# Performance work log

Hardware: AMD Instinct MI355X
Metric: run time of the kernel (lower is better)

## Reference

```python
import jax, jax.numpy as jnp
import numpy as np

EMBED_DIM = 768
NUM_HEADS = 12
HEAD_DIM = EMBED_DIM // NUM_HEADS


def setup_inputs() -> dict:
    key = jax.random.key(0)
    k_x, k_qkv_w, k_qkv_b, k_pw, k_pb = jax.random.split(key, 5)
    B, S = 16, 1024
    scale = 1.0 / np.sqrt(EMBED_DIM)
    return {
        "x": jax.random.normal(k_x, (B, S, EMBED_DIM), dtype=jnp.float32),
        "qkv_w": jax.random.normal(k_qkv_w, (EMBED_DIM, 3 * EMBED_DIM), dtype=jnp.float32) * scale,
        "qkv_b": jax.random.normal(k_qkv_b, (3 * EMBED_DIM,), dtype=jnp.float32) * 0.02,
        "proj_w": jax.random.normal(k_pw, (EMBED_DIM, EMBED_DIM), dtype=jnp.float32) * scale,
        "proj_b": jax.random.normal(k_pb, (EMBED_DIM,), dtype=jnp.float32) * 0.02,
    }


def reference(x, qkv_w, qkv_b, proj_w, proj_b):
    B, S, E = x.shape
    H, D = NUM_HEADS, HEAD_DIM
    qkv = x @ qkv_w + qkv_b                      # [B, S, 3E]
    qkv = qkv.reshape(B, S, 3, H, D)
    qkv = jnp.transpose(qkv, (2, 0, 3, 1, 4))    # [3, B, H, S, D]
    q, k, v = qkv[0], qkv[1], qkv[2]
    scores = jnp.einsum("bhqd,bhkd->bhqk", q, k) / jnp.sqrt(jnp.float32(D))
    probs = jax.nn.softmax(scores, axis=-1)      # dropout is identity in eval
    attn = jnp.einsum("bhqk,bhkd->bhqd", probs, v)
    attn = jnp.transpose(attn, (0, 2, 1, 3)).reshape(B, S, E)
    return attn @ proj_w + proj_b
```

## Files before the change

### kernel.cpp

```cpp
#include <hip/hip_runtime.h>
#include <hip/hip_bf16.h>

typedef unsigned short u16;
typedef short s16x8 __attribute__((ext_vector_type(8)));
typedef float f32x4 __attribute__((ext_vector_type(4)));

#define EMB 768
#define NH 12
#define HD 64
#define BB 16
#define SS 1024
#define MTOK (BB*SS)
#define NQKV (3*EMB)
#define QSZ ((size_t)BB*NH*SS*HD)

#define GLOBAL_AS const __attribute__((address_space(1))) void*
#define LDS_AS __attribute__((address_space(3))) void*

#if __has_builtin(__builtin_amdgcn_exp2f)
#define EXP2(x) __builtin_amdgcn_exp2f(x)
#else
#define EXP2(x) exp2f(x)
#endif

__device__ __forceinline__ u16 f2bf(float f){
  unsigned u = __float_as_uint(f);
  u += 0x7FFFu + ((u >> 16) & 1u);
  return (u16)(u >> 16);
}
__device__ __forceinline__ u16 f2bf_trunc(float f){
  return (u16)(__float_as_uint(f) >> 16);
}
__device__ __forceinline__ f32x4 mfma16(s16x8 a, s16x8 b, f32x4 c){
  return __builtin_amdgcn_mfma_f32_16x16x32_bf16(a, b, c, 0, 0, 0);
}

__global__ __launch_bounds__(256) void convert_f32_bf16(
    const float4* __restrict__ in, ushort4* __restrict__ out, int n4){
  int i = blockIdx.x * 256 + threadIdx.x;
  if(i < n4){
    float4 f = in[i];
    ushort4 o;
    o.x = f2bf(f.x); o.y = f2bf(f.y); o.z = f2bf(f.z); o.w = f2bf(f.w);
    out[i] = o;
  }
}

__global__ void transpose_conv(const float* __restrict__ in, u16* __restrict__ out,
                               int R, int C){
  __shared__ u16 tile[32][33];
  int bx = blockIdx.x * 32, by = blockIdx.y * 32;
  int tx = threadIdx.x & 31, ty = threadIdx.x >> 5;
  #pragma unroll
  for(int i = 0; i < 32; i += 8)
    tile[ty + i][tx] = f2bf(in[(size_t)(by + ty + i) * C + bx + tx]);
  __syncthreads();
  #pragma unroll
  for(int i = 0; i < 32; i += 8)
    out[(size_t)(bx + ty + i) * R + by + tx] = tile[tx][ty + i];
}

template<int MODE>
__global__ __launch_bounds__(256) void gemm_kernel(
    const u16* __restrict__ A, const u16* __restrict__ Bt,
    const float* __restrict__ bias,
    void* __restrict__ out0, u16* __restrict__ out1, u16* __restrict__ out2){
  const int K = 768;
  __shared__ u16 As[2][128*64];
  __shared__ u16 Bs[2][128*64];
  int tid = threadIdx.x;
  int m0 = blockIdx.y * 128, n0 = blockIdx.x * 128;
  int w = tid >> 6, lane = tid & 63, quad = lane >> 4, l15 = lane & 15;
  int wm = (w >> 1) * 64, wn = (w & 1) * 64;
  int rr = lane >> 3;
  int cp = lane & 7;
  f32x4 acc[4][4] = {};

  auto stage = [&](int p, int k0){
    #pragma unroll
    for(int it = 0; it < 4; ++it){
      int ci = it * 4 + w;
      int r  = ci * 8 + rr;
      int gc = (cp ^ (r & 7)) * 8;
      __builtin_amdgcn_global_load_lds(
          (GLOBAL_AS)(A + (size_t)(m0 + r) * K + k0 + gc),
          (LDS_AS)(As[p] + ci * 512 + lane * 8), 16, 0, 0);
      __builtin_amdgcn_global_load_lds(
          (GLOBAL_AS)(Bt + (size_t)(n0 + r) * K + k0 + gc),
          (LDS_AS)(Bs[p] + ci * 512 + lane * 8), 16, 0, 0);
    }
  };

  stage(0, 0);
  int p = 0;
  for(int k0 = 0; k0 < K; k0 += 64){
    __syncthreads();
    if(k0 + 64 < K) stage(p ^ 1, k0 + 64);
    #pragma unroll
    for(int kk = 0; kk < 2; kk++){
      s16x8 a[4], b[4];
      int ch = ((kk * 4 + quad) ^ (l15 & 7)) * 8;
      #pragma unroll
      for(int i = 0; i < 4; i++){
        a[i] = *(const s16x8*)&As[p][(wm + i*16 + l15) * 64 + ch];
        b[i] = *(const s16x8*)&Bs[p][(wn + i*16 + l15) * 64 + ch];
      }
      #pragma unroll
      for(int mt = 0; mt < 4; mt++)
        #pragma unroll
        for(int nt = 0; nt < 4; nt++)
          acc[mt][nt] = mfma16(a[mt], b[nt], acc[mt][nt]);
    }
    p ^= 1;
  }

  #pragma unroll
  for(int mt = 0; mt < 4; mt++){
    #pragma unroll
    for(int nt = 0; nt < 4; nt++){
      int n = n0 + wn + nt*16 + l15;
      float bv = bias[n];
      #pragma unroll
      for(int r = 0; r < 4; r++){
        int m = m0 + wm + mt*16 + quad*4 + r;
        float v = acc[mt][nt][r] + bv;
        if(MODE == 1){
          ((float*)out0)[(size_t)m * EMB + n] = v;
        } else {
          u16 hv = f2bf(v);
          int which = n / EMB, rem = n - which * EMB;
          int h = rem >> 6, d = rem & 63;
          int b = m >> 10, s = m & 1023;
          size_t bh = (size_t)(b * NH + h);
          if(which == 0)      ((u16*)out0)[(bh * SS + s) * HD + d] = hv;
          else if(which == 1) out1[(bh * SS + s) * HD + d] = hv;
          else                out2[(bh * HD + d) * SS + s] = hv;
        }
      }
    }
  }
}

__global__ __launch_bounds__(256) void attn_kernel(
    const u16* __restrict__ Qws, const u16* __restrict__ Kws,
    const u16* __restrict__ Vtws, u16* __restrict__ attn){
  __shared__ u16 Ks[2][64*64];
  __shared__ u16 Vs[2][64*64];
  __shared__ __align__(16) u16 Ps[4][2][16][76];
  int tid = threadIdx.x;
  int w = tid >> 6, lane = tid & 63, quad = lane >> 4, l15 = lane & 15;
  int bh = blockIdx.x;
  int b = bh / NH, h = bh - b * NH;
  int q0 = blockIdx.y * 128 + w * 32;
  const u16* Qbase = Qws  + (size_t)bh * SS * HD;
  const u16* Kbase = Kws  + (size_t)bh * SS * HD;
  const u16* Vbase = Vtws + (size_t)bh * HD * SS;

  s16x8 aq[2][2];
  #pragma unroll
  for(int m = 0; m < 2; m++){
    int qrow = q0 + m*16 + l15;
    #pragma unroll
    for(int kk = 0; kk < 2; kk++)
      aq[m][kk] = *(const s16x8*)(Qbase + (size_t)qrow * HD + kk*32 + quad*8);
  }

  f32x4 o[2][4] = {};
  float psum[2][4] = {};
  const float C1 = 0.125f * 1.44269504f;
  const float C0 = -30.0f * 1.44269504f;

  int krr = lane >> 3, kcp = lane & 7;

  auto stageKV = [&](int p, int kt){
    #pragma unroll
    for(int it = 0; it < 2; ++it){
      int ins = it * 4 + w;
      int r   = ins * 8 + krr;
      int gck = (kcp ^ (r & 7)) * 8;
      __builtin_amdgcn_global_load_lds(
          (GLOBAL_AS)(Kbase + (size_t)(kt*64 + r) * HD + gck),
          (LDS_AS)(Ks[p] + ins * 512 + lane * 8), 16, 0, 0);
      __builtin_amdgcn_global_load_lds(
          (GLOBAL_AS)(Vbase + (size_t)r * SS + kt*64 + gck),
          (LDS_AS)(Vs[p] + ins * 512 + lane * 8), 16, 0, 0);
    }
  };

  stageKV(0, 0);
  int p = 0;
  for(int kt = 0; kt < 16; ++kt){
    __syncthreads();
    if(kt < 15) stageKV(p ^ 1, kt + 1);

    #pragma unroll
    for(int nt = 0; nt < 4; ++nt){
      s16x8 bk[2];
      #pragma unroll
      for(int kk = 0; kk < 2; kk++){
        int ch = ((kk*4 + quad) ^ (l15 & 7)) * 8;
        bk[kk] = *(const s16x8*)&Ks[p][(nt*16 + l15) * 64 + ch];
      }
      #pragma unroll
      for(int m = 0; m < 2; m++){
        f32x4 z = {};
        z = mfma16(aq[m][0], bk[0], z);
        z = mfma16(aq[m][1], bk[1], z);
        #pragma unroll
        for(int r = 0; r < 4; r++){
          float pv = EXP2(z[r] * C1 + C0);
          psum[m][r] += pv;
          Ps[w][m][quad*4 + r][nt*16 + l15] = f2bf_trunc(pv);
        }
      }
    }
    #pragma unroll
    for(int k4 = 0; k4 < 2; k4++){
      s16x8 pa[2];
      #pragma unroll
      for(int m = 0; m < 2; m++)
        pa[m] = *(const s16x8*)&Ps[w][m][l15][k4*32 + quad*8];
      #pragma unroll
      for(int nt = 0; nt < 4; nt++){
        int ch = ((k4*4 + quad) ^ (l15 & 7)) * 8;
        s16x8 vb = *(const s16x8*)&Vs[p][(nt*16 + l15) * 64 + ch];
        #pragma unroll
        for(int m = 0; m < 2; m++)
          o[m][nt] = mfma16(pa[m], vb, o[m][nt]);
      }
    }
    p ^= 1;
  }

  #pragma unroll
  for(int m = 0; m < 2; m++){
    #pragma unroll
    for(int r = 0; r < 4; r++){
      float s = psum[m][r];
      s += __shfl_xor(s, 1, 64);
      s += __shfl_xor(s, 2, 64);
      s += __shfl_xor(s, 4, 64);
      s += __shfl_xor(s, 8, 64);
      float inv = 1.0f / s;
      int srow = q0 + m*16 + quad*4 + r;
      size_t base = ((size_t)(b * SS + srow)) * EMB + h * HD;
      #pragma unroll
      for(int nt = 0; nt < 4; nt++)
        attn[base + nt*16 + l15] = f2bf(o[m][nt][r] * inv);
    }
  }
}

extern "C" void kernel_launch(void* const* d_in, const int* in_sizes, int n_in,
                              void* d_out, int out_size, void* d_ws, size_t ws_size,
                              hipStream_t stream){
  const float* x      = (const float*)d_in[0];
  const float* qkv_w  = (const float*)d_in[1];
  const float* qkv_b  = (const float*)d_in[2];
  const float* proj_w = (const float*)d_in[3];
  const float* proj_b = (const float*)d_in[4];

  char* ws = (char*)d_ws;
  u16* qkv_wT  = (u16*)ws; ws += (size_t)NQKV * EMB * 2;
  u16* proj_wT = (u16*)ws; ws += (size_t)EMB * EMB * 2;
  u16* x_bf = (u16*)ws; ws += QSZ * 2;
  u16* Qws  = (u16*)ws; ws += QSZ * 2;
  u16* Kws  = (u16*)ws; ws += QSZ * 2;
  u16* Vtws = (u16*)ws; ws += QSZ * 2;
  u16* attn = x_bf;

  int n4 = (int)(QSZ / 4);
  convert_f32_bf16<<<(n4 + 255) / 256, 256, 0, stream>>>(
      (const float4*)x, (ushort4*)x_bf, n4);
  transpose_conv<<<dim3(NQKV/32, EMB/32), 256, 0, stream>>>(qkv_w, qkv_wT, EMB, NQKV);
  transpose_conv<<<dim3(EMB/32, EMB/32), 256, 0, stream>>>(proj_w, proj_wT, EMB, EMB);
  gemm_kernel<0><<<dim3(NQKV/128, MTOK/128), 256, 0, stream>>>(
      x_bf, qkv_wT, qkv_b, Qws, Kws, Vtws);
  attn_kernel<<<dim3(BB*NH, SS/128), 256, 0, stream>>>(Qws, Kws, Vtws, attn);
  gemm_kernel<1><<<dim3(EMB/128, MTOK/128), 256, 0, stream>>>(
      attn, proj_wT, proj_b, d_out, nullptr, nullptr);
}
```

Baseline: 328.8 us.

## Rewrite GEMM as 256x256 tiles with 4-stage LDS pipeline and XCD remap

Replaces the 128x128 double-buffered GEMM with a 256x256 tile, 512-thread kernel using a 4-deep ring of K=32 LDS stages and split A/B prefetch interleaved with MFMA halves under explicit waitcnt, barriers and setprio. The block index is remapped to group workgroups by XCD for better L2 reuse, and the LDS swizzle changes for the narrower K chunk. The aim is to raise arithmetic intensity and hide global-load latency in both QKV and projection GEMMs. The price is larger tiles that yield fewer workgroups (e.g. 192 for the projection GEMM), higher register pressure, and hand-tuned wait counts that must be exactly right.

```diff
diff --git a/kernel.cpp b/kernel.cpp
--- a/kernel.cpp
+++ b/kernel.cpp
@@ -61,80 +61,116 @@
 }
 
 template<int MODE>
-__global__ __launch_bounds__(256) void gemm_kernel(
+__global__ __launch_bounds__(512, 2) void gemm_kernel(
     const u16* __restrict__ A, const u16* __restrict__ Bt,
     const float* __restrict__ bias,
     void* __restrict__ out0, u16* __restrict__ out1, u16* __restrict__ out2){
-  const int K = 768;
-  __shared__ u16 As[2][128*64];
-  __shared__ u16 Bs[2][128*64];
+  const int K = 768, NS = 24;
+  __shared__ u16 As[4][256*32];
+  __shared__ u16 Bs[4][256*32];
   int tid = threadIdx.x;
-  int m0 = blockIdx.y * 128, n0 = blockIdx.x * 128;
   int w = tid >> 6, lane = tid & 63, quad = lane >> 4, l15 = lane & 15;
-  int wm = (w >> 1) * 64, wn = (w & 1) * 64;
-  int rr = lane >> 3;
-  int cp = lane & 7;
-  f32x4 acc[4][4] = {};
-
-  auto stage = [&](int p, int k0){
-    #pragma unroll
-    for(int it = 0; it < 4; ++it){
-      int ci = it * 4 + w;
-      int r  = ci * 8 + rr;
-      int gc = (cp ^ (r & 7)) * 8;
-      __builtin_amdgcn_global_load_lds(
-          (GLOBAL_AS)(A + (size_t)(m0 + r) * K + k0 + gc),
-          (LDS_AS)(As[p] + ci * 512 + lane * 8), 16, 0, 0);
-      __builtin_amdgcn_global_load_lds(
-          (GLOBAL_AS)(Bt + (size_t)(n0 + r) * K + k0 + gc),
-          (LDS_AS)(Bs[p] + ci * 512 + lane * 8), 16, 0, 0);
-    }
+  int wm = (w >> 2) * 128, wn = (w & 3) * 64;
+
+  int gx = gridDim.x;
+  int nwg = gx * gridDim.y;
+  int L = blockIdx.y * gx + blockIdx.x;
+  int nl = (L & 7) * (nwg >> 3) + (L >> 3);
+  int m0 = (nl / gx) * 256, n0 = (nl % gx) * 256;
+
+  f32x4 acc[8][4] = {};
+
+  int ci0 = tid, ci1 = 512 + tid;
+  int row0 = ci0 >> 2, row1 = ci1 >> 2;
+  int cc0 = (ci0 & 3) ^ ((row0 ^ (row0 >> 2)) & 3);
+  int cc1 = (ci1 & 3) ^ ((row1 ^ (row1 >> 2)) & 3);
+  const u16* a0 = A  + (size_t)(m0 + row0) * K + cc0 * 8;
+  const u16* a1 = A  + (size_t)(m0 + row1) * K + cc1 * 8;
+  const u16* b0 = Bt + (size_t)(n0 + row0) * K + cc0 * 8;
+  const u16* b1 = Bt + (size_t)(n0 + row1) * K + cc1 * 8;
+
+  auto stageA = [&](int s){
+    int r = s & 3, k0 = s * 32;
+    __builtin_amdgcn_global_load_lds((GLOBAL_AS)(a0 + k0),
+        (LDS_AS)(As[r] + ci0 * 8), 16, 0, 0);
+    __builtin_amdgcn_global_load_lds((GLOBAL_AS)(a1 + k0),
+        (LDS_AS)(As[r] + ci1 * 8), 16, 0, 0);
   };
-
-  stage(0, 0);
-  int p = 0;
-  for(int k0 = 0; k0 < K; k0 += 64){
-    __syncthreads();
-    if(k0 + 64 < K) stage(p ^ 1, k0 + 64);
-    #pragma unroll
-    for(int kk = 0; kk < 2; kk++){
-      s16x8 a[4], b[4];
-      int ch = ((kk * 4 + quad) ^ (l15 & 7)) * 8;
-      #pragma unroll
-      for(int i = 0; i < 4; i++){
-        a[i] = *(const s16x8*)&As[p][(wm + i*16 + l15) * 64 + ch];
-        b[i] = *(const s16x8*)&Bs[p][(wn + i*16 + l15) * 64 + ch];
-      }
-      #pragma unroll
-      for(int mt = 0; mt < 4; mt++)
-        #pragma unroll
-        for(int nt = 0; nt < 4; nt++)
-          acc[mt][nt] = mfma16(a[mt], b[nt], acc[mt][nt]);
-    }
-    p ^= 1;
-  }
-
-  #pragma unroll
-  for(int mt = 0; mt < 4; mt++){
-    #pragma unroll
-    for(int nt = 0; nt < 4; nt++){
+  auto stageB = [&](int s){
+    int r = s & 3, k0 = s * 32;
+    __builtin_amdgcn_global_load_lds((GLOBAL_AS)(b0 + k0),
+        (LDS_AS)(Bs[r] + ci0 * 8), 16, 0, 0);
+    __builtin_amdgcn_global_load_lds((GLOBAL_AS)(b1 + k0),
+        (LDS_AS)(Bs[r] + ci1 * 8), 16, 0, 0);
+  };
+
+  int chk  = (quad ^ ((l15 ^ (l15 >> 2)) & 3)) * 8;
+  int aoff = (wm + l15) * 32 + chk;
+  int boff = (wn + l15) * 32 + chk;
+
+  stageA(0); stageB(0); stageA(1); stageB(1);
+  asm volatile("s_waitcnt vmcnt(4)" ::: "memory");
+  __builtin_amdgcn_s_barrier();
+
+  #pragma unroll
+  for(int s = 0; s < NS; ++s){
+    int r = s & 3;
+    s16x8 a[4], b[4];
+    #pragma unroll
+    for(int nt = 0; nt < 4; ++nt) b[nt] = *(const s16x8*)&Bs[r][boff + nt*512];
+    #pragma unroll
+    for(int mt = 0; mt < 4; ++mt) a[mt] = *(const s16x8*)&As[r][aoff + mt*512];
+    if(s + 2 < NS) stageA(s + 2);
+    __builtin_amdgcn_s_barrier();
+    asm volatile("s_waitcnt lgkmcnt(0)" ::: "memory");
+    __builtin_amdgcn_sched_barrier(0);
+    __builtin_amdgcn_s_setprio(1);
+    #pragma unroll
+    for(int mt = 0; mt < 4; ++mt)
+      #pragma unroll
+      for(int nt = 0; nt < 4; ++nt)
+        acc[mt][nt] = mfma16(a[mt], b[nt], acc[mt][nt]);
+    __builtin_amdgcn_s_setprio(0);
+    __builtin_amdgcn_s_barrier();
+    #pragma unroll
+    for(int mt = 0; mt < 4; ++mt) a[mt] = *(const s16x8*)&As[r][aoff + (mt+4)*512];
+    if(s + 2 < NS) stageB(s + 2);
+    __builtin_amdgcn_s_barrier();
+    asm volatile("s_waitcnt lgkmcnt(0)" ::: "memory");
+    __builtin_amdgcn_sched_barrier(0);
+    __builtin_amdgcn_s_setprio(1);
+    #pragma unroll
+    for(int mt = 0; mt < 4; ++mt)
+      #pragma unroll
+      for(int nt = 0; nt < 4; ++nt)
+        acc[mt+4][nt] = mfma16(a[mt], b[nt], acc[mt+4][nt]);
+    __builtin_amdgcn_s_setprio(0);
+    if(s < NS - 2)       asm volatile("s_waitcnt vmcnt(4)" ::: "memory");
+    else if(s == NS - 2) asm volatile("s_waitcnt vmcnt(0)" ::: "memory");
+    __builtin_amdgcn_s_barrier();
+  }
+
+  #pragma unroll
+  for(int mt = 0; mt < 8; ++mt){
+    #pragma unroll
+    for(int nt = 0; nt < 4; ++nt){
       int n = n0 + wn + nt*16 + l15;
       float bv = bias[n];
       #pragma unroll
-      for(int r = 0; r < 4; r++){
-        int m = m0 + wm + mt*16 + quad*4 + r;
-        float v = acc[mt][nt][r] + bv;
+      for(int r2 = 0; r2 < 4; ++r2){
+        int m = m0 + wm + mt*16 + quad*4 + r2;
+        float v = acc[mt][nt][r2] + bv;
         if(MODE == 1){
           ((float*)out0)[(size_t)m * EMB + n] = v;
         } else {
           u16 hv = f2bf(v);
           int which = n / EMB, rem = n - which * EMB;
           int h = rem >> 6, d = rem & 63;
-          int b = m >> 10, s = m & 1023;
-          size_t bh = (size_t)(b * NH + h);
-          if(which == 0)      ((u16*)out0)[(bh * SS + s) * HD + d] = hv;
-          else if(which == 1) out1[(bh * SS + s) * HD + d] = hv;
-          else                out2[(bh * HD + d) * SS + s] = hv;
+          int bb = m >> 10, ss = m & 1023;
+          size_t bh = (size_t)(bb * NH + h);
+          if(which == 0)      ((u16*)out0)[(bh * SS + ss) * HD + d] = hv;
+          else if(which == 1) out1[(bh * SS + ss) * HD + d] = hv;
+          else                out2[(bh * HD + d) * SS + ss] = hv;
         }
       }
     }
@@ -274,9 +310,9 @@
       (const float4*)x, (ushort4*)x_bf, n4);
   transpose_conv<<<dim3(NQKV/32, EMB/32), 256, 0, stream>>>(qkv_w, qkv_wT, EMB, NQKV);
   transpose_conv<<<dim3(EMB/32, EMB/32), 256, 0, stream>>>(proj_w, proj_wT, EMB, EMB);
-  gemm_kernel<0><<<dim3(NQKV/128, MTOK/128), 256, 0, stream>>>(
+  gemm_kernel<0><<<dim3(NQKV/256, MTOK/256), 512, 0, stream>>>(
       x_bf, qkv_wT, qkv_b, Qws, Kws, Vtws);
   attn_kernel<<<dim3(BB*NH, SS/128), 256, 0, stream>>>(Qws, Kws, Vtws, attn);
-  gemm_kernel<1><<<dim3(EMB/128, MTOK/128), 256, 0, stream>>>(
+  gemm_kernel<1><<<dim3(EMB/256, MTOK/256), 512, 0, stream>>>(
       attn, proj_wT, proj_b, d_out, nullptr, nullptr);
 }
```

New measurement: 335.4 us. Within noise of the previous version (+2.0%).
